# Kernel tuning notes

Hardware: AMD Instinct MI355X
Metric: run time of the kernel (lower is better)

The kernel has to match this reference:

```python
import jax, jax.numpy as jnp
import numpy as np

B, S = 4096, 256
D = 32  # output_size // 4


def setup_inputs() -> dict:
    key = jax.random.key(0)
    ks = jax.random.split(key, 32)
    # continuous features
    cont_p = jax.random.normal(ks[0], (B, S, 3), dtype=jnp.float32)
    cont_c = jax.random.normal(ks[1], (B, S, 2), dtype=jnp.float32)
    # categorical features, per-column vocab sizes from Embedding tables
    vocabs_p = [2, 2, 2, 11, 34]
    cat_p = jnp.stack([
        jax.random.randint(ks[2 + i], (B, S), 0, v, dtype=jnp.int32)
        for i, v in enumerate(vocabs_p)], axis=2)
    vocabs_c = [19, 31]
    cat_c = jnp.stack([
        jax.random.randint(ks[7 + i], (B, S), 0, v, dtype=jnp.int32)
        for i, v in enumerate(vocabs_c)], axis=2)
    lengths = jax.random.randint(ks[9], (B,), 1, S + 1, dtype=jnp.int32)

    def lin(k, fan_in, fan_out):
        bound = 1.0 / np.sqrt(fan_in)
        kw, kb = jax.random.split(k)
        w = jax.random.uniform(kw, (fan_in, fan_out), jnp.float32, -bound, bound)
        b = jax.random.uniform(kb, (fan_out,), jnp.float32, -bound, bound)
        return w, b

    w_p1, b_p1 = lin(ks[10], 3, D)
    w_p2, b_p2 = lin(ks[11], D, D)
    w_c1, b_c1 = lin(ks[12], 2, D)
    w_c2, b_c2 = lin(ks[13], D, D)
    emb_gender = jax.random.normal(ks[14], (2, D), dtype=jnp.float32)
    emb_korean = jax.random.normal(ks[15], (2, D), dtype=jnp.float32)
    emb_primary = jax.random.normal(ks[16], (2, D), dtype=jnp.float32)
    emb_job = jax.random.normal(ks[17], (11, D), dtype=jnp.float32)
    emb_rep = jax.random.normal(ks[18], (34, D), dtype=jnp.float32)
    emb_place = jax.random.normal(ks[19], (19, D), dtype=jnp.float32)
    emb_add = jax.random.normal(ks[20], (31, D), dtype=jnp.float32)
    w_fc1, b_fc1 = lin(ks[21], 128, 64)
    w_fc2, b_fc2 = lin(ks[22], 64, 2)

    return dict(cont_p=cont_p, cont_c=cont_c, cat_p=cat_p, cat_c=cat_c,
                lengths=lengths,
                w_p1=w_p1, b_p1=b_p1, w_p2=w_p2, b_p2=b_p2,
                w_c1=w_c1, b_c1=b_c1, w_c2=w_c2, b_c2=b_c2,
                emb_gender=emb_gender, emb_korean=emb_korean,
                emb_primary=emb_primary, emb_job=emb_job, emb_rep=emb_rep,
                emb_place=emb_place, emb_add=emb_add,
                w_fc1=w_fc1, b_fc1=b_fc1, w_fc2=w_fc2, b_fc2=b_fc2)


def reference(cont_p, cont_c, cat_p, cat_c, lengths,
              w_p1, b_p1, w_p2, b_p2, w_c1, b_c1, w_c2, b_c2,
              emb_gender, emb_korean, emb_primary, emb_job, emb_rep,
              emb_place, emb_add, w_fc1, b_fc1, w_fc2, b_fc2):
    # small per-token MLPs on continuous features -> [B,S,D]
    hp = jax.nn.relu(cont_p @ w_p1 + b_p1) @ w_p2 + b_p2
    hc = jax.nn.relu(cont_c @ w_c1 + b_c1) @ w_c2 + b_c2
    # multi-table embedding lookups, averaged per group -> [B,S,D]
    ep = (emb_gender[cat_p[:, :, 0]] + emb_korean[cat_p[:, :, 1]] +
          emb_primary[cat_p[:, :, 2]] + emb_job[cat_p[:, :, 3]] +
          emb_rep[cat_p[:, :, 4]]) / 5.0
    ec = (emb_place[cat_c[:, :, 0]] + emb_add[cat_c[:, :, 1]]) / 2.0
    # concat order matches torch: (cat_p, cat_c, cont_p, cont_c) -> [B,S,128]
    x = jnp.concatenate([ep, ec, hp, hc], axis=2)
    # ragged mean pool over first lengths[i] positions (masked segment mean)
    mask = (jnp.arange(x.shape[1])[None, :] < lengths[:, None])
    pooled = jnp.sum(x * mask[:, :, None], axis=1) / lengths[:, None].astype(x.dtype)
    # head: relu(fc1) -> relu(fc2); dropout p=0.0 is identity
    h = jax.nn.relu(pooled @ w_fc1 + b_fc1)
    return jax.nn.relu(h @ w_fc2 + b_fc2)
```

## Files before the change

### kernel.cpp

```cpp
#include <hip/hip_runtime.h>


#define BDIM 64

__global__ __launch_bounds__(BDIM)
void mlpreg_kernel(const float* __restrict__ cont_p,
                   const float* __restrict__ cont_c,
                   const int* __restrict__ cat_p,
                   const int* __restrict__ cat_c,
                   const int* __restrict__ lengths,
                   const float* __restrict__ w_p1, const float* __restrict__ b_p1,
                   const float* __restrict__ w_p2, const float* __restrict__ b_p2,
                   const float* __restrict__ w_c1, const float* __restrict__ b_c1,
                   const float* __restrict__ w_c2, const float* __restrict__ b_c2,
                   const float* __restrict__ emb_g,  const float* __restrict__ emb_k,
                   const float* __restrict__ emb_pr, const float* __restrict__ emb_j,
                   const float* __restrict__ emb_r,  const float* __restrict__ emb_pl,
                   const float* __restrict__ emb_a,
                   const float* __restrict__ w_fc1, const float* __restrict__ b_fc1,
                   const float* __restrict__ w_fc2, const float* __restrict__ b_fc2,
                   float* __restrict__ out)
{
    constexpr int S = 256;
    __shared__ float sP[2][S * 3];
    __shared__ float sC[2][S * 2];
    __shared__ int   hist[2][96];
    __shared__ float sPacc[2][64];
    __shared__ float sPool[2][128];

    const int lane = threadIdx.x;
    const int b0 = blockIdx.x * 2, b1 = b0 + 1;

    int L0 = lengths[b0]; L0 = (L0 < 1) ? 1 : (L0 > S ? S : L0);
    int L1 = lengths[b1]; L1 = (L1 < 1) ? 1 : (L1 > S ? S : L1);
    const float L0f = (float)L0, L1f = (float)L1;
    const float invL0 = 1.0f / L0f, invL1 = 1.0f / L1f;

    { int i = lane;            ((int*)hist)[i] = 0;
      i += 64;                 ((int*)hist)[i] = 0;
      i += 64;                 ((int*)hist)[i] = 0; }

    const int ch = lane & 31, h = lane >> 5;
    const float wp0 = w_p1[ch], wp1 = w_p1[32 + ch], wp2 = w_p1[64 + ch], bp = b_p1[ch];
    const float wc0 = w_c1[ch], wc1 = w_c1[32 + ch], bc = b_c1[ch];

    {
        const float4* gp0 = (const float4*)(cont_p + (size_t)b0 * (S * 3));
        const float4* gp1 = (const float4*)(cont_p + (size_t)b1 * (S * 3));
        const float4* gc0 = (const float4*)(cont_c + (size_t)b0 * (S * 2));
        const float4* gc1 = (const float4*)(cont_c + (size_t)b1 * (S * 2));
        const int n0 = (3 * L0 + 3) >> 2, n1 = (3 * L1 + 3) >> 2;
        const int m0 = (2 * L0 + 3) >> 2, m1 = (2 * L1 + 3) >> 2;
        for (int i = lane; i < n0; i += 64) *(float4*)&sP[0][4 * i] = gp0[i];
        for (int i = lane; i < n1; i += 64) *(float4*)&sP[1][4 * i] = gp1[i];
        for (int i = lane; i < m0; i += 64) *(float4*)&sC[0][4 * i] = gc0[i];
        for (int i = lane; i < m1; i += 64) *(float4*)&sC[1][4 * i] = gc1[i];
    }

    int sg0 = 0, sk0 = 0, sp0 = 0, sg1 = 0, sk1 = 0, sp1 = 0;
    {
        const int*  kp0 = cat_p + (size_t)b0 * (S * 5);
        const int*  kp1 = cat_p + (size_t)b1 * (S * 5);
        const int2* kc0 = (const int2*)(cat_c + (size_t)b0 * (S * 2));
        const int2* kc1 = (const int2*)(cat_c + (size_t)b1 * (S * 2));
        #pragma unroll 2
        for (int t = lane; t < L0; t += 64) {
            int v0 = kp0[5 * t], v1 = kp0[5 * t + 1], v2 = kp0[5 * t + 2],
                v3 = kp0[5 * t + 3], v4 = kp0[5 * t + 4];
            int2 q = kc0[t];
            sg0 += v0; sk0 += v1; sp0 += v2;
            atomicAdd(&hist[0][v3], 1);
            atomicAdd(&hist[0][11 + v4], 1);
            atomicAdd(&hist[0][45 + q.x], 1);
            atomicAdd(&hist[0][64 + q.y], 1);
        }
        #pragma unroll 2
        for (int t = lane; t < L1; t += 64) {
            int v0 = kp1[5 * t], v1 = kp1[5 * t + 1], v2 = kp1[5 * t + 2],
                v3 = kp1[5 * t + 3], v4 = kp1[5 * t + 4];
            int2 q = kc1[t];
            sg1 += v0; sk1 += v1; sp1 += v2;
            atomicAdd(&hist[1][v3], 1);
            atomicAdd(&hist[1][11 + v4], 1);
            atomicAdd(&hist[1][45 + q.x], 1);
            atomicAdd(&hist[1][64 + q.y], 1);
        }
    }
    #pragma unroll
    for (int d = 32; d; d >>= 1) {
        sg0 += __shfl_xor(sg0, d); sk0 += __shfl_xor(sk0, d); sp0 += __shfl_xor(sp0, d);
        sg1 += __shfl_xor(sg1, d); sk1 += __shfl_xor(sk1, d); sp1 += __shfl_xor(sp1, d);
    }
    __syncthreads();

    {
        const int   Lr   = h ? L1 : L0;
        const float invr = h ? invL1 : invL0;
        const float* tp = sP[h];
        const float* tc = sC[h];
        float aP = 0.f, aC = 0.f;
        #pragma unroll 4
        for (int t = 0; t < Lr; ++t) {
            float c0 = tp[3 * t], c1 = tp[3 * t + 1], c2 = tp[3 * t + 2];
            float2 d2 = *(const float2*)&tc[2 * t];
            aP += fmaxf(fmaf(c0, wp0, fmaf(c1, wp1, fmaf(c2, wp2, bp))), 0.f);
            aC += fmaxf(fmaf(d2.x, wc0, fmaf(d2.y, wc1, bc)), 0.f);
        }
        sPacc[h][ch]      = aP * invr;
        sPacc[h][32 + ch] = aC * invr;
    }
    __syncthreads();

    if (h == 0) {
        float g0 = emb_g[ch],  g1 = emb_g[32 + ch];
        float k0 = emb_k[ch],  k1 = emb_k[32 + ch];
        float p0 = emb_pr[ch], p1 = emb_pr[32 + ch];
        float fg0 = (float)sg0, fk0 = (float)sk0, fp0 = (float)sp0;
        float fg1 = (float)sg1, fk1 = (float)sk1, fp1 = (float)sp1;
        float A0 = fmaf(L0f - fg0, g0, fg0 * g1) + fmaf(L0f - fk0, k0, fk0 * k1)
                 + fmaf(L0f - fp0, p0, fp0 * p1);
        float A1 = fmaf(L1f - fg1, g0, fg1 * g1) + fmaf(L1f - fk1, k0, fk1 * k1)
                 + fmaf(L1f - fp1, p0, fp1 * p1);
        #pragma unroll
        for (int r = 0; r < 11; ++r) {
            float w = emb_j[r * 32 + ch];
            A0 = fmaf((float)hist[0][r], w, A0);
            A1 = fmaf((float)hist[1][r], w, A1);
        }
        #pragma unroll
        for (int r = 0; r < 34; ++r) {
            float w = emb_r[r * 32 + ch];
            A0 = fmaf((float)hist[0][11 + r], w, A0);
            A1 = fmaf((float)hist[1][11 + r], w, A1);
        }
        sPool[0][ch] = A0 * (invL0 * 0.2f);
        sPool[1][ch] = A1 * (invL1 * 0.2f);

        float v0 = b_p2[ch], v1 = v0;
        #pragma unroll
        for (int k = 0; k < 32; ++k) {
            float w = w_p2[k * 32 + ch];
            v0 = fmaf(sPacc[0][k], w, v0);
            v1 = fmaf(sPacc[1][k], w, v1);
        }
        sPool[0][64 + ch] = v0;
        sPool[1][64 + ch] = v1;
    } else {
        float A0 = 0.f, A1 = 0.f;
        #pragma unroll
        for (int r = 0; r < 19; ++r) {
            float w = emb_pl[r * 32 + ch];
            A0 = fmaf((float)hist[0][45 + r], w, A0);
            A1 = fmaf((float)hist[1][45 + r], w, A1);
        }
        #pragma unroll
        for (int r = 0; r < 31; ++r) {
            float w = emb_a[r * 32 + ch];
            A0 = fmaf((float)hist[0][64 + r], w, A0);
            A1 = fmaf((float)hist[1][64 + r], w, A1);
        }
        sPool[0][32 + ch] = A0 * (invL0 * 0.5f);
        sPool[1][32 + ch] = A1 * (invL1 * 0.5f);

        float v0 = b_c2[ch], v1 = v0;
        #pragma unroll
        for (int k = 0; k < 32; ++k) {
            float w = w_c2[k * 32 + ch];
            v0 = fmaf(sPacc[0][32 + k], w, v0);
            v1 = fmaf(sPacc[1][32 + k], w, v1);
        }
        sPool[0][96 + ch] = v0;
        sPool[1][96 + ch] = v1;
    }
    __syncthreads();

    {
        const int o = lane;
        float x0 = b_fc1[o], y0 = 0.f;
        float x1 = x0,       y1 = 0.f;
        #pragma unroll 8
        for (int k = 0; k < 128; k += 2) {
            float wa = w_fc1[(size_t)k * 64 + o];
            float wb = w_fc1[(size_t)(k + 1) * 64 + o];
            float u0 = sPool[0][k], u1 = sPool[0][k + 1];
            float s0 = sPool[1][k], s1 = sPool[1][k + 1];
            x0 = fmaf(u0, wa, x0); y0 = fmaf(u1, wb, y0);
            x1 = fmaf(s0, wa, x1); y1 = fmaf(s1, wb, y1);
        }
        float h0 = fmaxf(x0 + y0, 0.f);
        float h1 = fmaxf(x1 + y1, 0.f);
        float wa = w_fc2[2 * o], wb = w_fc2[2 * o + 1];
        float q00 = h0 * wa, q01 = h0 * wb, q10 = h1 * wa, q11 = h1 * wb;
        #pragma unroll
        for (int d = 32; d; d >>= 1) {
            q00 += __shfl_xor(q00, d); q01 += __shfl_xor(q01, d);
            q10 += __shfl_xor(q10, d); q11 += __shfl_xor(q11, d);
        }
        if (lane == 0) {
            float bb0 = b_fc2[0], bb1 = b_fc2[1];
            float4 o4;
            o4.x = fmaxf(q00 + bb0, 0.f);
            o4.y = fmaxf(q01 + bb1, 0.f);
            o4.z = fmaxf(q10 + bb0, 0.f);
            o4.w = fmaxf(q11 + bb1, 0.f);
            *(float4*)&out[(size_t)b0 * 2] = o4;
        }
    }
}

extern "C" void kernel_launch(void* const* d_in, const int* in_sizes, int n_in,
                              void* d_out, int out_size, void* d_ws, size_t ws_size,
                              hipStream_t stream) {
    const float* cont_p = (const float*)d_in[0];
    const float* cont_c = (const float*)d_in[1];
    const int*   cat_p  = (const int*)d_in[2];
    const int*   cat_c  = (const int*)d_in[3];
    const int*   lens   = (const int*)d_in[4];
    const float* w_p1   = (const float*)d_in[5];
    const float* b_p1   = (const float*)d_in[6];
    const float* w_p2   = (const float*)d_in[7];
    const float* b_p2   = (const float*)d_in[8];
    const float* w_c1   = (const float*)d_in[9];
    const float* b_c1   = (const float*)d_in[10];
    const float* w_c2   = (const float*)d_in[11];
    const float* b_c2   = (const float*)d_in[12];
    const float* emb_g  = (const float*)d_in[13];
    const float* emb_k  = (const float*)d_in[14];
    const float* emb_pr = (const float*)d_in[15];
    const float* emb_j  = (const float*)d_in[16];
    const float* emb_r  = (const float*)d_in[17];
    const float* emb_pl = (const float*)d_in[18];
    const float* emb_a  = (const float*)d_in[19];
    const float* w_fc1  = (const float*)d_in[20];
    const float* b_fc1  = (const float*)d_in[21];
    const float* w_fc2  = (const float*)d_in[22];
    const float* b_fc2  = (const float*)d_in[23];
    float* out = (float*)d_out;

    hipLaunchKernelGGL(mlpreg_kernel, dim3(2048), dim3(BDIM), 0, stream,
                       cont_p, cont_c, cat_p, cat_c, lens,
                       w_p1, b_p1, w_p2, b_p2, w_c1, b_c1, w_c2, b_c2,
                       emb_g, emb_k, emb_pr, emb_j, emb_r, emb_pl, emb_a,
                       w_fc1, b_fc1, w_fc2, b_fc2, out);
}
```

Baseline: 139.9 us.

## Keep continuous features in registers and broadcast via readlane instead of LDS staging

Continuous features are loaded directly into per-lane registers (4 tokens per lane per row) and broadcast with readlane in the per-token MLP loop, removing the LDS staging buffers and their sync. The three binary category sums are packed into one integer for a single shuffle reduction. Histogram-embedding and second-layer matvecs are split across both half-waves with shuffle combines, and fc1 reads pooled inputs via readlane instead of LDS. This trades LDS traffic for scalar readlane serialization, and the register arrays raise register pressure.

```diff
diff --git a/kernel.cpp b/kernel.cpp
--- a/kernel.cpp
+++ b/kernel.cpp
@@ -2,6 +2,10 @@
 
 
 #define BDIM 64
+
+__device__ __forceinline__ float rlf(float v, int l) {
+    return __int_as_float(__builtin_amdgcn_readlane(__float_as_int(v), l));
+}
 
 __global__ __launch_bounds__(BDIM)
 void mlpreg_kernel(const float* __restrict__ cont_p,
@@ -22,10 +26,8 @@
                    float* __restrict__ out)
 {
     constexpr int S = 256;
-    __shared__ float sP[2][S * 3];
-    __shared__ float sC[2][S * 2];
     __shared__ int   hist[2][96];
-    __shared__ float sPacc[2][64];
+    __shared__ float pacc[2][64];
     __shared__ float sPool[2][128];
 
     const int lane = threadIdx.x;
@@ -36,161 +38,195 @@
     const float L0f = (float)L0, L1f = (float)L1;
     const float invL0 = 1.0f / L0f, invL1 = 1.0f / L1f;
 
-    { int i = lane;            ((int*)hist)[i] = 0;
-      i += 64;                 ((int*)hist)[i] = 0;
-      i += 64;                 ((int*)hist)[i] = 0; }
+    ((int*)hist)[lane]       = 0;
+    ((int*)hist)[64 + lane]  = 0;
+    ((int*)hist)[128 + lane] = 0;
 
     const int ch = lane & 31, h = lane >> 5;
     const float wp0 = w_p1[ch], wp1 = w_p1[32 + ch], wp2 = w_p1[64 + ch], bp = b_p1[ch];
     const float wc0 = w_c1[ch], wc1 = w_c1[32 + ch], bc = b_c1[ch];
 
-    {
-        const float4* gp0 = (const float4*)(cont_p + (size_t)b0 * (S * 3));
-        const float4* gp1 = (const float4*)(cont_p + (size_t)b1 * (S * 3));
-        const float4* gc0 = (const float4*)(cont_c + (size_t)b0 * (S * 2));
-        const float4* gc1 = (const float4*)(cont_c + (size_t)b1 * (S * 2));
-        const int n0 = (3 * L0 + 3) >> 2, n1 = (3 * L1 + 3) >> 2;
-        const int m0 = (2 * L0 + 3) >> 2, m1 = (2 * L1 + 3) >> 2;
-        for (int i = lane; i < n0; i += 64) *(float4*)&sP[0][4 * i] = gp0[i];
-        for (int i = lane; i < n1; i += 64) *(float4*)&sP[1][4 * i] = gp1[i];
-        for (int i = lane; i < m0; i += 64) *(float4*)&sC[0][4 * i] = gc0[i];
-        for (int i = lane; i < m1; i += 64) *(float4*)&sC[1][4 * i] = gc1[i];
-    }
-
-    int sg0 = 0, sk0 = 0, sp0 = 0, sg1 = 0, sk1 = 0, sp1 = 0;
-    {
-        const int*  kp0 = cat_p + (size_t)b0 * (S * 5);
-        const int*  kp1 = cat_p + (size_t)b1 * (S * 5);
-        const int2* kc0 = (const int2*)(cat_c + (size_t)b0 * (S * 2));
-        const int2* kc1 = (const int2*)(cat_c + (size_t)b1 * (S * 2));
-        #pragma unroll 2
-        for (int t = lane; t < L0; t += 64) {
-            int v0 = kp0[5 * t], v1 = kp0[5 * t + 1], v2 = kp0[5 * t + 2],
-                v3 = kp0[5 * t + 3], v4 = kp0[5 * t + 4];
-            int2 q = kc0[t];
-            sg0 += v0; sk0 += v1; sp0 += v2;
-            atomicAdd(&hist[0][v3], 1);
-            atomicAdd(&hist[0][11 + v4], 1);
-            atomicAdd(&hist[0][45 + q.x], 1);
-            atomicAdd(&hist[0][64 + q.y], 1);
-        }
-        #pragma unroll 2
-        for (int t = lane; t < L1; t += 64) {
-            int v0 = kp1[5 * t], v1 = kp1[5 * t + 1], v2 = kp1[5 * t + 2],
-                v3 = kp1[5 * t + 3], v4 = kp1[5 * t + 4];
-            int2 q = kc1[t];
-            sg1 += v0; sk1 += v1; sp1 += v2;
-            atomicAdd(&hist[1][v3], 1);
-            atomicAdd(&hist[1][11 + v4], 1);
-            atomicAdd(&hist[1][45 + q.x], 1);
-            atomicAdd(&hist[1][64 + q.y], 1);
-        }
-    }
-    #pragma unroll
-    for (int d = 32; d; d >>= 1) {
-        sg0 += __shfl_xor(sg0, d); sk0 += __shfl_xor(sk0, d); sp0 += __shfl_xor(sp0, d);
-        sg1 += __shfl_xor(sg1, d); sk1 += __shfl_xor(sk1, d); sp1 += __shfl_xor(sp1, d);
-    }
+    float cp[2][4][3], cd[2][4][2];
+    {
+        const float* gp[2] = { cont_p + (size_t)b0 * (S * 3), cont_p + (size_t)b1 * (S * 3) };
+        const float* gc[2] = { cont_c + (size_t)b0 * (S * 2), cont_c + (size_t)b1 * (S * 2) };
+        const int Ls[2] = { L0, L1 };
+        #pragma unroll
+        for (int r = 0; r < 2; ++r) {
+            #pragma unroll
+            for (int bt = 0; bt < 4; ++bt) {
+                int t = bt * 64 + lane;
+                int tc = (t < Ls[r]) ? t : (Ls[r] - 1);
+                cp[r][bt][0] = gp[r][3 * tc];
+                cp[r][bt][1] = gp[r][3 * tc + 1];
+                cp[r][bt][2] = gp[r][3 * tc + 2];
+                float2 dd = *(const float2*)&gc[r][2 * tc];
+                cd[r][bt][0] = dd.x; cd[r][bt][1] = dd.y;
+            }
+        }
+    }
+
+    int pk[2] = { 0, 0 };
+    {
+        const int*  kp[2] = { cat_p + (size_t)b0 * (S * 5), cat_p + (size_t)b1 * (S * 5) };
+        const int2* kc[2] = { (const int2*)(cat_c + (size_t)b0 * (S * 2)),
+                              (const int2*)(cat_c + (size_t)b1 * (S * 2)) };
+        const int Ls[2] = { L0, L1 };
+        #pragma unroll
+        for (int r = 0; r < 2; ++r) {
+            #pragma unroll
+            for (int bt = 0; bt < 4; ++bt) {
+                int t = bt * 64 + lane;
+                if (t < Ls[r]) {
+                    int v0 = kp[r][5 * t], v1 = kp[r][5 * t + 1], v2 = kp[r][5 * t + 2],
+                        v3 = kp[r][5 * t + 3], v4 = kp[r][5 * t + 4];
+                    int2 q = kc[r][t];
+                    pk[r] += v0 + (v1 << 10) + (v2 << 20);
+                    atomicAdd(&hist[r][v3], 1);
+                    atomicAdd(&hist[r][11 + v4], 1);
+                    atomicAdd(&hist[r][46 + q.x], 1);
+                    atomicAdd(&hist[r][65 + q.y], 1);
+                }
+            }
+        }
+        #pragma unroll
+        for (int d = 32; d; d >>= 1) {
+            pk[0] += __shfl_xor(pk[0], d);
+            pk[1] += __shfl_xor(pk[1], d);
+        }
+    }
+    const float sg0 = (float)(pk[0] & 1023), sk0 = (float)((pk[0] >> 10) & 1023),
+                sp0 = (float)(pk[0] >> 20);
+    const float sg1 = (float)(pk[1] & 1023), sk1 = (float)((pk[1] >> 10) & 1023),
+                sp1 = (float)(pk[1] >> 20);
+
+    float accP0 = 0.f, accC0 = 0.f, accP1 = 0.f, accC1 = 0.f;
+    {
+        const int Ls[2] = { L0, L1 };
+        #pragma unroll
+        for (int r = 0; r < 2; ++r) {
+            #pragma unroll
+            for (int bt = 0; bt < 4; ++bt) {
+                int base = bt * 64;
+                if (base < Ls[r]) {
+                    int cnt = Ls[r] - base; if (cnt > 64) cnt = 64;
+                    #pragma unroll 8
+                    for (int s = 0; s < cnt; ++s) {
+                        float c0 = rlf(cp[r][bt][0], s);
+                        float c1 = rlf(cp[r][bt][1], s);
+                        float c2 = rlf(cp[r][bt][2], s);
+                        float d0 = rlf(cd[r][bt][0], s);
+                        float d1 = rlf(cd[r][bt][1], s);
+                        float vP = fmaf(c0, wp0, fmaf(c1, wp1, fmaf(c2, wp2, bp)));
+                        float vC = fmaf(d0, wc0, fmaf(d1, wc1, bc));
+                        if (r == 0) { accP0 += fmaxf(vP, 0.f); accC0 += fmaxf(vC, 0.f); }
+                        else        { accP1 += fmaxf(vP, 0.f); accC1 += fmaxf(vC, 0.f); }
+                    }
+                }
+            }
+        }
+    }
+    accP0 *= invL0; accC0 *= invL0; accP1 *= invL1; accC1 *= invL1;
+    pacc[0][lane] = (lane < 32) ? accP0 : accC0;
+    pacc[1][lane] = (lane < 32) ? accP1 : accC1;
     __syncthreads();
 
-    {
-        const int   Lr   = h ? L1 : L0;
-        const float invr = h ? invL1 : invL0;
-        const float* tp = sP[h];
-        const float* tc = sC[h];
-        float aP = 0.f, aC = 0.f;
-        #pragma unroll 4
-        for (int t = 0; t < Lr; ++t) {
-            float c0 = tp[3 * t], c1 = tp[3 * t + 1], c2 = tp[3 * t + 2];
-            float2 d2 = *(const float2*)&tc[2 * t];
-            aP += fmaxf(fmaf(c0, wp0, fmaf(c1, wp1, fmaf(c2, wp2, bp))), 0.f);
-            aC += fmaxf(fmaf(d2.x, wc0, fmaf(d2.y, wc1, bc)), 0.f);
-        }
-        sPacc[h][ch]      = aP * invr;
-        sPacc[h][32 + ch] = aC * invr;
-    }
-    __syncthreads();
-
-    if (h == 0) {
+    float A0, A1;
+    {
         float g0 = emb_g[ch],  g1 = emb_g[32 + ch];
         float k0 = emb_k[ch],  k1 = emb_k[32 + ch];
-        float p0 = emb_pr[ch], p1 = emb_pr[32 + ch];
-        float fg0 = (float)sg0, fk0 = (float)sk0, fp0 = (float)sp0;
-        float fg1 = (float)sg1, fk1 = (float)sk1, fp1 = (float)sp1;
-        float A0 = fmaf(L0f - fg0, g0, fg0 * g1) + fmaf(L0f - fk0, k0, fk0 * k1)
-                 + fmaf(L0f - fp0, p0, fp0 * p1);
-        float A1 = fmaf(L1f - fg1, g0, fg1 * g1) + fmaf(L1f - fk1, k0, fk1 * k1)
-                 + fmaf(L1f - fp1, p0, fp1 * p1);
-        #pragma unroll
-        for (int r = 0; r < 11; ++r) {
-            float w = emb_j[r * 32 + ch];
-            A0 = fmaf((float)hist[0][r], w, A0);
-            A1 = fmaf((float)hist[1][r], w, A1);
-        }
-        #pragma unroll
-        for (int r = 0; r < 34; ++r) {
-            float w = emb_r[r * 32 + ch];
-            A0 = fmaf((float)hist[0][11 + r], w, A0);
-            A1 = fmaf((float)hist[1][11 + r], w, A1);
-        }
-        sPool[0][ch] = A0 * (invL0 * 0.2f);
-        sPool[1][ch] = A1 * (invL1 * 0.2f);
-
-        float v0 = b_p2[ch], v1 = v0;
-        #pragma unroll
-        for (int k = 0; k < 32; ++k) {
+        float q0 = emb_pr[ch], q1 = emb_pr[32 + ch];
+        float bin0 = fmaf(L0f - sg0, g0, sg0 * g1) + fmaf(L0f - sk0, k0, sk0 * k1)
+                   + fmaf(L0f - sp0, q0, sp0 * q1);
+        float bin1 = fmaf(L1f - sg1, g0, sg1 * g1) + fmaf(L1f - sk1, k0, sk1 * k1)
+                   + fmaf(L1f - sp1, q0, sp1 * q1);
+        A0 = h ? 0.f : bin0;
+        A1 = h ? 0.f : bin1;
+        #pragma unroll
+        for (int i = 0; i < 23; ++i) {
+            int b = 2 * i + h;
+            float c0 = (float)hist[0][b], c1 = (float)hist[1][b];
+            int br = (b < 44) ? b : 44;
+            const float* tp = (b < 11) ? (emb_j + b * 32) : (emb_r + (br - 11) * 32);
+            float w = tp[ch];
+            A0 = fmaf(c0, w, A0);
+            A1 = fmaf(c1, w, A1);
+        }
+        A0 += __shfl_down(A0, 32);
+        A1 += __shfl_down(A1, 32);
+    }
+    float E0 = 0.f, E1 = 0.f;
+    {
+        #pragma unroll
+        for (int i = 0; i < 25; ++i) {
+            int b = 46 + 2 * i + h;
+            float c0 = (float)hist[0][b], c1 = (float)hist[1][b];
+            const float* tp = (b < 65) ? (emb_pl + (b - 46) * 32) : (emb_a + (b - 65) * 32);
+            float w = tp[ch];
+            E0 = fmaf(c0, w, E0);
+            E1 = fmaf(c1, w, E1);
+        }
+        E0 += __shfl_down(E0, 32);
+        E1 += __shfl_down(E1, 32);
+    }
+
+    float vp0, vp1, vc0, vc1;
+    {
+        float bb = b_p2[ch];
+        vp0 = h ? 0.f : bb; vp1 = vp0;
+        #pragma unroll
+        for (int i = 0; i < 16; ++i) {
+            int k = h * 16 + i;
             float w = w_p2[k * 32 + ch];
-            v0 = fmaf(sPacc[0][k], w, v0);
-            v1 = fmaf(sPacc[1][k], w, v1);
-        }
-        sPool[0][64 + ch] = v0;
-        sPool[1][64 + ch] = v1;
-    } else {
-        float A0 = 0.f, A1 = 0.f;
-        #pragma unroll
-        for (int r = 0; r < 19; ++r) {
-            float w = emb_pl[r * 32 + ch];
-            A0 = fmaf((float)hist[0][45 + r], w, A0);
-            A1 = fmaf((float)hist[1][45 + r], w, A1);
-        }
-        #pragma unroll
-        for (int r = 0; r < 31; ++r) {
-            float w = emb_a[r * 32 + ch];
-            A0 = fmaf((float)hist[0][64 + r], w, A0);
-            A1 = fmaf((float)hist[1][64 + r], w, A1);
-        }
-        sPool[0][32 + ch] = A0 * (invL0 * 0.5f);
-        sPool[1][32 + ch] = A1 * (invL1 * 0.5f);
-
-        float v0 = b_c2[ch], v1 = v0;
-        #pragma unroll
-        for (int k = 0; k < 32; ++k) {
+            vp0 = fmaf(pacc[0][k], w, vp0);
+            vp1 = fmaf(pacc[1][k], w, vp1);
+        }
+        vp0 += __shfl_down(vp0, 32);
+        vp1 += __shfl_down(vp1, 32);
+        float bb2 = b_c2[ch];
+        vc0 = h ? 0.f : bb2; vc1 = vc0;
+        #pragma unroll
+        for (int i = 0; i < 16; ++i) {
+            int k = h * 16 + i;
             float w = w_c2[k * 32 + ch];
-            v0 = fmaf(sPacc[0][32 + k], w, v0);
-            v1 = fmaf(sPacc[1][32 + k], w, v1);
-        }
-        sPool[0][96 + ch] = v0;
-        sPool[1][96 + ch] = v1;
+            vc0 = fmaf(pacc[0][32 + k], w, vc0);
+            vc1 = fmaf(pacc[1][32 + k], w, vc1);
+        }
+        vc0 += __shfl_down(vc0, 32);
+        vc1 += __shfl_down(vc1, 32);
+    }
+    if (lane < 32) {
+        sPool[0][ch]      = A0 * (invL0 * 0.2f);
+        sPool[1][ch]      = A1 * (invL1 * 0.2f);
+        sPool[0][32 + ch] = E0 * (invL0 * 0.5f);
+        sPool[1][32 + ch] = E1 * (invL1 * 0.5f);
+        sPool[0][64 + ch] = vp0;  sPool[1][64 + ch] = vp1;
+        sPool[0][96 + ch] = vc0;  sPool[1][96 + ch] = vc1;
     }
     __syncthreads();
 
     {
-        const int o = lane;
-        float x0 = b_fc1[o], y0 = 0.f;
-        float x1 = x0,       y1 = 0.f;
-        #pragma unroll 8
-        for (int k = 0; k < 128; k += 2) {
-            float wa = w_fc1[(size_t)k * 64 + o];
-            float wb = w_fc1[(size_t)(k + 1) * 64 + o];
-            float u0 = sPool[0][k], u1 = sPool[0][k + 1];
-            float s0 = sPool[1][k], s1 = sPool[1][k + 1];
-            x0 = fmaf(u0, wa, x0); y0 = fmaf(u1, wb, y0);
-            x1 = fmaf(s0, wa, x1); y1 = fmaf(s1, wb, y1);
-        }
-        float h0 = fmaxf(x0 + y0, 0.f);
-        float h1 = fmaxf(x1 + y1, 0.f);
-        float wa = w_fc2[2 * o], wb = w_fc2[2 * o + 1];
-        float q00 = h0 * wa, q01 = h0 * wb, q10 = h1 * wa, q11 = h1 * wb;
+        float r0a = sPool[0][lane], r0b = sPool[0][64 + lane];
+        float r1a = sPool[1][lane], r1b = sPool[1][64 + lane];
+        float x0 = b_fc1[lane], x1 = x0, y0 = 0.f, y1 = 0.f;
+        #pragma unroll
+        for (int k = 0; k < 64; k += 2) {
+            float wa = w_fc1[(size_t)k * 64 + lane];
+            float wb = w_fc1[(size_t)(k + 1) * 64 + lane];
+            x0 = fmaf(rlf(r0a, k), wa, x0);  y0 = fmaf(rlf(r0a, k + 1), wb, y0);
+            x1 = fmaf(rlf(r1a, k), wa, x1);  y1 = fmaf(rlf(r1a, k + 1), wb, y1);
+        }
+        #pragma unroll
+        for (int k = 0; k < 64; k += 2) {
+            float wa = w_fc1[(size_t)(64 + k) * 64 + lane];
+            float wb = w_fc1[(size_t)(65 + k) * 64 + lane];
+            x0 = fmaf(rlf(r0b, k), wa, x0);  y0 = fmaf(rlf(r0b, k + 1), wb, y0);
+            x1 = fmaf(rlf(r1b, k), wa, x1);  y1 = fmaf(rlf(r1b, k + 1), wb, y1);
+        }
+        float h0v = fmaxf(x0 + y0, 0.f);
+        float h1v = fmaxf(x1 + y1, 0.f);
+        float wa = w_fc2[2 * lane], wb = w_fc2[2 * lane + 1];
+        float q00 = h0v * wa, q01 = h0v * wb, q10 = h1v * wa, q11 = h1v * wb;
         #pragma unroll
         for (int d = 32; d; d >>= 1) {
             q00 += __shfl_xor(q00, d); q01 += __shfl_xor(q01, d);
```

After: 167.0 us. 19.4% more time.
